# Kernel tuning notes

Measured on AMD Instinct MI355X. Metric: run time of the kernel, lower is better.

## Reference

```python
import jax, jax.numpy as jnp
import numpy as np

EMBD = 1024
N_HEADS = 16
DK = EMBD // N_HEADS


def setup_inputs() -> dict:
    key = jax.random.key(0)
    ks = jax.random.split(key, 5)
    B, T = 2, 2048
    scale = 1.0 / np.sqrt(EMBD)
    x = jax.random.normal(ks[0], (B, T, EMBD), dtype=jnp.float32)
    W_qkv = jax.random.normal(ks[1], (EMBD, 3 * EMBD), dtype=jnp.float32) * scale
    b_qkv = jnp.zeros((3 * EMBD,), dtype=jnp.float32)
    W_proj = jax.random.normal(ks[2], (EMBD, EMBD), dtype=jnp.float32) * scale
    b_proj = jnp.zeros((EMBD,), dtype=jnp.float32)
    return {"x": x, "W_qkv": W_qkv, "b_qkv": b_qkv, "W_proj": W_proj, "b_proj": b_proj}


def reference(x, W_qkv, b_qkv, W_proj, b_proj):
    B, T, C = x.shape
    qkv = x @ W_qkv + b_qkv                      # [B, T, 3C]
    q, k, v = jnp.split(qkv, 3, axis=-1)
    # [B, H, T, dk]
    q = q.reshape(B, T, N_HEADS, DK).transpose(0, 2, 1, 3)
    k = k.reshape(B, T, N_HEADS, DK).transpose(0, 2, 1, 3)
    v = v.reshape(B, T, N_HEADS, DK).transpose(0, 2, 1, 3)
    att = jnp.einsum('bhqd,bhkd->bhqk', q, k) / np.sqrt(DK).astype(np.float32)
    causal = jnp.triu(jnp.full((T, T), -jnp.inf, dtype=att.dtype), k=1)
    att = jax.nn.softmax(att + causal, axis=-1)  # dropout p=0.0 -> identity
    y = jnp.einsum('bhqk,bhkd->bhqd', att, v)    # [B, H, T, dk]
    y = y.transpose(0, 2, 1, 3).reshape(B, T, C)
    y = y @ W_proj + b_proj
    return (y, (k, v))
```

## Files before the change

### kernel.cpp

```cpp
#include <hip/hip_runtime.h>
#include <hip/hip_bf16.h>

#define B_   2
#define T_   2048
#define C_   1024
#define H_   16
#define DK_  64

typedef __bf16 bf16x8 __attribute__((ext_vector_type(8)));
typedef float  f32x4  __attribute__((ext_vector_type(4)));
typedef unsigned short u16;
typedef u16 u16x4 __attribute__((ext_vector_type(4)));
typedef u16 u16x8 __attribute__((ext_vector_type(8)));

static __device__ __forceinline__ u16 f2bf(float f) {
    unsigned u = __float_as_uint(f);
    u += 0x7fffu + ((u >> 16) & 1u);
    return (u16)(u >> 16);
}
static __device__ __forceinline__ float bf2f(u16 h) {
    return __uint_as_float(((unsigned)h) << 16);
}

static __device__ __forceinline__ void async16(void* l, const void* g) {
    __builtin_amdgcn_global_load_lds(
        (const __attribute__((address_space(1))) unsigned int*)g,
        (__attribute__((address_space(3))) unsigned int*)l, 16, 0, 0);
}

__global__ __launch_bounds__(256) void pack_a_hl(const float* __restrict__ src, char* __restrict__ dst) {
    const int mt = blockIdx.x, kt = blockIdx.y, t = threadIdx.x;
    const int r = t >> 1, half = t & 1;
    const float* s = src + (size_t)(mt * 128 + r) * 1024 + kt * 32 + half * 16;
    float f[16];
    #pragma unroll
    for (int i = 0; i < 4; ++i) *(float4*)&f[i * 4] = ((const float4*)s)[i];
    u16 hi[16] __attribute__((aligned(16))), lo[16] __attribute__((aligned(16)));
    #pragma unroll
    for (int e = 0; e < 16; ++e) { hi[e] = f2bf(f[e]); lo[e] = f2bf(f[e] - bf2f(hi[e])); }
    char* tb = dst + ((size_t)mt * 32 + kt) * 16384;
    const int sw = (r & 7) << 4;
    #pragma unroll
    for (int j = 0; j < 2; ++j) {
        int g = half * 2 + j;
        *(u16x8*)(tb + ((r * 128 + g * 16) ^ sw))      = *(u16x8*)&hi[j * 8];
        *(u16x8*)(tb + ((r * 128 + 64 + g * 16) ^ sw)) = *(u16x8*)&lo[j * 8];
    }
}

__global__ __launch_bounds__(256) void pack_a_s(const float* __restrict__ src, char* __restrict__ dst) {
    const int mt = blockIdx.x, kt = blockIdx.y, t = threadIdx.x;
    const int r = t >> 1, half = t & 1;
    const float* s = src + (size_t)(mt * 128 + r) * 1024 + kt * 64 + half * 32;
    float f[32];
    #pragma unroll
    for (int i = 0; i < 8; ++i) *(float4*)&f[i * 4] = ((const float4*)s)[i];
    u16 hv[32] __attribute__((aligned(16)));
    #pragma unroll
    for (int e = 0; e < 32; ++e) hv[e] = f2bf(f[e]);
    char* tb = dst + ((size_t)mt * 16 + kt) * 16384;
    const int sw = (r & 7) << 4;
    #pragma unroll
    for (int j = 0; j < 4; ++j) {
        int g = half * 4 + j;
        *(u16x8*)(tb + ((r * 128 + g * 16) ^ sw)) = *(u16x8*)&hv[j * 8];
    }
}

template <int BKT>
__global__ __launch_bounds__(256) void pack_bt_hl(const float* __restrict__ W, char* __restrict__ dst,
                                                  int N, int nkt) {
    __shared__ float Ls[BKT][132];
    const int nt = blockIdx.x, kt = blockIdx.y, t = threadIdx.x;
    #pragma unroll
    for (int p = 0; p < BKT / 32; ++p) {
        int kr = p * 32 + (t >> 3), c8 = t & 7;
        const float* s = W + (size_t)(kt * BKT + kr) * N + nt * 128 + c8 * 16;
        #pragma unroll
        for (int i = 0; i < 4; ++i) *(float4*)&Ls[kr][c8 * 16 + i * 4] = ((const float4*)s)[i];
    }
    __syncthreads();
    const int nr = t >> 1, half = t & 1;
    constexpr int KH = BKT / 2;
    constexpr int ROWB = BKT * 4;
    constexpr int TILEB = 128 * ROWB;
    char* tb = dst + ((size_t)nt * nkt + kt) * TILEB;
    u16 hi[KH] __attribute__((aligned(16))), lo[KH] __attribute__((aligned(16)));
    #pragma unroll
    for (int e = 0; e < KH; ++e) {
        float x = Ls[half * KH + e][nr];
        hi[e] = f2bf(x); lo[e] = f2bf(x - bf2f(hi[e]));
    }
    const int sw = (nr & 7) << 4;
    #pragma unroll
    for (int j = 0; j < KH / 8; ++j) {
        int g = half * (KH / 8) + j;
        *(u16x8*)(tb + ((nr * ROWB + g * 16) ^ sw))            = *(u16x8*)&hi[j * 8];
        *(u16x8*)(tb + ((nr * ROWB + ROWB / 2 + g * 16) ^ sw)) = *(u16x8*)&lo[j * 8];
    }
}

__global__ __launch_bounds__(256) void kv_pack(
    const float* __restrict__ k_in, const float* __restrict__ v_in,
    char* __restrict__ kp, char* __restrict__ vp)
{
    __shared__ float Ls[64][68];
    const int bh = blockIdx.x, kt = blockIdx.y, t = threadIdx.x;
    const float* Kb = k_in + (size_t)bh * T_ * DK_ + (size_t)kt * 64 * DK_;
    const float* Vb = v_in + (size_t)bh * T_ * DK_ + (size_t)kt * 64 * DK_;
    char* ktb = kp + ((size_t)bh * 32 + kt) * 16384;
    char* vtb = vp + ((size_t)bh * 32 + kt) * 16384;
    const int row = t >> 2, qtr = t & 3;

    {
        float f[16];
        #pragma unroll
        for (int i = 0; i < 4; ++i)
            *(float4*)&f[i * 4] = ((const float4*)(Kb + (size_t)row * 64 + qtr * 16))[i];
        u16 hi[16] __attribute__((aligned(16))), lo[16] __attribute__((aligned(16)));
        #pragma unroll
        for (int e = 0; e < 16; ++e) { hi[e] = f2bf(f[e]); lo[e] = f2bf(f[e] - bf2f(hi[e])); }
        const int sw = (row & 7) << 4;
        *(u16x8*)(ktb + ((row * 128 + qtr * 32) ^ sw))             = *(u16x8*)&hi[0];
        *(u16x8*)(ktb + ((row * 128 + qtr * 32 + 16) ^ sw))        = *(u16x8*)&hi[8];
        *(u16x8*)(ktb + 8192 + ((row * 128 + qtr * 32) ^ sw))      = *(u16x8*)&lo[0];
        *(u16x8*)(ktb + 8192 + ((row * 128 + qtr * 32 + 16) ^ sw)) = *(u16x8*)&lo[8];
    }

    #pragma unroll
    for (int i = 0; i < 4; ++i)
        *(float4*)&Ls[row][qtr * 16 + i * 4] = ((const float4*)(Vb + (size_t)row * 64 + qtr * 16))[i];
    __syncthreads();
    {
        const int dd = t >> 2, tc2 = t & 3;
        float f[16];
        #pragma unroll
        for (int k = 0; k < 16; ++k) f[k] = Ls[tc2 * 16 + k][dd];
        u16 hi[16] __attribute__((aligned(16))), lo[16] __attribute__((aligned(16)));
        #pragma unroll
        for (int e = 0; e < 16; ++e) { hi[e] = f2bf(f[e]); lo[e] = f2bf(f[e] - bf2f(hi[e])); }
        const int sw = (dd & 7) << 4;
        *(u16x8*)(vtb + ((dd * 128 + tc2 * 32) ^ sw))             = *(u16x8*)&hi[0];
        *(u16x8*)(vtb + ((dd * 128 + tc2 * 32 + 16) ^ sw))        = *(u16x8*)&hi[8];
        *(u16x8*)(vtb + 8192 + ((dd * 128 + tc2 * 32) ^ sw))      = *(u16x8*)&lo[0];
        *(u16x8*)(vtb + 8192 + ((dd * 128 + tc2 * 32 + 16) ^ sw)) = *(u16x8*)&lo[8];
    }
}

__global__ __launch_bounds__(256, 2) void qkv_gemm_bf16(
    const char* __restrict__ xp, const char* __restrict__ wqp,
    const float* __restrict__ bqkv,
    float* __restrict__ qy, float* __restrict__ k_out, float* __restrict__ v_out)
{
    __shared__ __align__(16) char Alds[16384];
    __shared__ __align__(16) char Blds[16384];
    const int mt = blockIdx.x, nt = blockIdx.y;
    const int t = threadIdx.x, lane = t & 63, w = t >> 6;
    const int g = lane >> 4, r15 = lane & 15;
    const int wm = w >> 1, wn = w & 1;

    int aoff[4][2], boff[4][2];
    #pragma unroll
    for (int s = 0; s < 4; ++s) {
        int ar = wm * 64 + s * 16 + r15, sa = (ar & 7) << 4;
        aoff[s][0] = (ar * 128 + g * 16) ^ sa;
        aoff[s][1] = (ar * 128 + 64 + g * 16) ^ sa;
        int br = wn * 64 + s * 16 + r15, sb = (br & 7) << 4;
        boff[s][0] = (br * 128 + g * 16) ^ sb;
        boff[s][1] = (br * 128 + 64 + g * 16) ^ sb;
    }

    f32x4 acc[4][4];
    #pragma unroll
    for (int i = 0; i < 4; ++i)
        #pragma unroll
        for (int j = 0; j < 4; ++j) acc[i][j] = (f32x4){0.f, 0.f, 0.f, 0.f};

    const char* Abase = xp + (size_t)mt * 32 * 16384 + w * 4096 + lane * 16;
    const char* Bbase = wqp + (size_t)nt * 32 * 16384 + w * 4096 + lane * 16;
    char* la = Alds + w * 4096;
    char* lb = Blds + w * 4096;

    for (int kt = 0; kt < 32; ++kt) {
        #pragma unroll
        for (int i = 0; i < 4; ++i) {
            async16(la + i * 1024, Abase + kt * 16384 + i * 1024);
            async16(lb + i * 1024, Bbase + kt * 16384 + i * 1024);
        }
        __syncthreads();
        bf16x8 af[4][2], bf[4][2];
        #pragma unroll
        for (int s = 0; s < 4; ++s) {
            af[s][0] = *(const bf16x8*)(Alds + aoff[s][0]);
            af[s][1] = *(const bf16x8*)(Alds + aoff[s][1]);
            bf[s][0] = *(const bf16x8*)(Blds + boff[s][0]);
            bf[s][1] = *(const bf16x8*)(Blds + boff[s][1]);
        }
        #pragma unroll
        for (int i = 0; i < 4; ++i)
            #pragma unroll
            for (int j = 0; j < 4; ++j) {
                acc[i][j] = __builtin_amdgcn_mfma_f32_16x16x32_bf16(af[i][0], bf[j][0], acc[i][j], 0, 0, 0);
                acc[i][j] = __builtin_amdgcn_mfma_f32_16x16x32_bf16(af[i][0], bf[j][1], acc[i][j], 0, 0, 0);
                acc[i][j] = __builtin_amdgcn_mfma_f32_16x16x32_bf16(af[i][1], bf[j][0], acc[i][j], 0, 0, 0);
            }
        __syncthreads();
    }

    const int n0 = nt * 128;
    const int sec = n0 >> 10;
    float* kv = (sec == 1) ? k_out : v_out;
    #pragma unroll
    for (int i = 0; i < 4; ++i) {
        int mbase = mt * 128 + wm * 64 + i * 16 + g * 4;
        #pragma unroll
        for (int j = 0; j < 4; ++j) {
            int n = n0 + wn * 64 + j * 16 + r15;
            float bias = bqkv[n];
            int c = n & 1023;
            #pragma unroll
            for (int r = 0; r < 4; ++r) {
                int m = mbase + r;
                int bb = m >> 11, tt = m & 2047;
                float val = acc[i][j][r] + bias;
                if (sec == 0)
                    qy[((size_t)bb * T_ + tt) * C_ + c] = val;
                else
                    kv[(((size_t)bb * H_ + (c >> 6)) * T_ + tt) * DK_ + (c & 63)] = val;
            }
        }
    }
}

__global__ __launch_bounds__(256, 2) void proj_gemm_bf16(
    const char* __restrict__ yap, const char* __restrict__ wpp,
    const float* __restrict__ bp, float* __restrict__ y)
{
    __shared__ __align__(16) char Alds[16384];
    __shared__ __align__(16) char Blds[32768];
    const int mt = blockIdx.x, nt = blockIdx.y;
    const int t = threadIdx.x, lane = t & 63, w = t >> 6;
    const int g = lane >> 4, r15 = lane & 15;
    const int wm = w >> 1, wn = w & 1;

    int aoff[4][2], boffh[4][2], boffl[4][2];
    #pragma unroll
    for (int s = 0; s < 4; ++s) {
        int ar = wm * 64 + s * 16 + r15, sa = (ar & 7) << 4;
        int br = wn * 64 + s * 16 + r15, sb = (br & 7) << 4;
        #pragma unroll
        for (int kk = 0; kk < 2; ++kk) {
            aoff[s][kk]  = (ar * 128 + (kk * 4 + g) * 16) ^ sa;
            boffh[s][kk] = (br * 256 + (kk * 4 + g) * 16) ^ sb;
            boffl[s][kk] = (br * 256 + 128 + (kk * 4 + g) * 16) ^ sb;
        }
    }

    f32x4 acc[4][4];
    #pragma unroll
    for (int i = 0; i < 4; ++i)
        #pragma unroll
        for (int j = 0; j < 4; ++j) acc[i][j] = (f32x4){0.f, 0.f, 0.f, 0.f};

    const char* Abase = yap + (size_t)mt * 16 * 16384 + w * 4096 + lane * 16;
    const char* Bbase = wpp + (size_t)nt * 16 * 32768 + w * 8192 + lane * 16;
    char* la = Alds + w * 4096;
    char* lb = Blds + w * 8192;

    for (int kt = 0; kt < 16; ++kt) {
        #pragma unroll
        for (int i = 0; i < 4; ++i)
            async16(la + i * 1024, Abase + kt * 16384 + i * 1024);
        #pragma unroll
        for (int i = 0; i < 8; ++i)
            async16(lb + i * 1024, Bbase + kt * 32768 + i * 1024);
        __syncthreads();
        #pragma unroll
        for (int kk = 0; kk < 2; ++kk) {
            bf16x8 af[4], bh[4], bl[4];
            #pragma unroll
            for (int s = 0; s < 4; ++s) {
                af[s] = *(const bf16x8*)(Alds + aoff[s][kk]);
                bh[s] = *(const bf16x8*)(Blds + boffh[s][kk]);
                bl[s] = *(const bf16x8*)(Blds + boffl[s][kk]);
            }
            #pragma unroll
            for (int i = 0; i < 4; ++i)
                #pragma unroll
                for (int j = 0; j < 4; ++j) {
                    acc[i][j] = __builtin_amdgcn_mfma_f32_16x16x32_bf16(af[i], bh[j], acc[i][j], 0, 0, 0);
                    acc[i][j] = __builtin_amdgcn_mfma_f32_16x16x32_bf16(af[i], bl[j], acc[i][j], 0, 0, 0);
                }
        }
        __syncthreads();
    }

    #pragma unroll
    for (int i = 0; i < 4; ++i) {
        int mbase = mt * 128 + wm * 64 + i * 16 + g * 4;
        #pragma unroll
        for (int j = 0; j < 4; ++j) {
            int n = nt * 128 + wn * 64 + j * 16 + r15;
            float bias = bp[n];
            #pragma unroll
            for (int r = 0; r < 4; ++r)
                y[(size_t)(mbase + r) * 1024 + n] = acc[i][j][r] + bias;
        }
    }
}

#define PS_H 0
#define PS_L 8192
#define KS_H 16384
#define KS_L 24576
#define VT_H 32768
#define VT_L 40960

__global__ __launch_bounds__(256) void attn_mfma_kernel(
    float* qyatt,
    const char* __restrict__ Kp,
    const char* __restrict__ Vp)
{
    __shared__ __align__(16) char lds[49152];

    const int bh   = blockIdx.x;
    const int qt   = 31 - (int)blockIdx.y;
    const int qb   = qt * 64;
    const int t    = threadIdx.x;
    const int lane = t & 63;
    const int w    = t >> 6;
    const int g    = lane >> 4;
    const int r15  = lane & 15;
    const int b    = bh >> 4, h = bh & 15;

    const float* Qb = qyatt + ((size_t)b * T_ + qb) * C_ + h * 64;

    #pragma unroll
    for (int di = 0; di < 4; ++di) {
        int fidx = di * 256 + t;
        int row  = fidx >> 4;
        int c4   = fidx & 15;
        float4 f = ((const float4*)(Qb + (size_t)row * C_))[c4];
        f.x *= 0.125f; f.y *= 0.125f; f.z *= 0.125f; f.w *= 0.125f;
        u16 h0 = f2bf(f.x), h1 = f2bf(f.y), h2 = f2bf(f.z), h3 = f2bf(f.w);
        u16 l0 = f2bf(f.x - bf2f(h0)), l1 = f2bf(f.y - bf2f(h1));
        u16 l2 = f2bf(f.z - bf2f(h2)), l3 = f2bf(f.w - bf2f(h3));
        int off = (row * 128 + c4 * 8) ^ ((row & 7) << 4);
        u16x4 hv = {h0, h1, h2, h3};
        u16x4 lv = {l0, l1, l2, l3};
        *(u16x4*)(lds + PS_H + off) = hv;
        *(u16x4*)(lds + PS_L + off) = lv;
    }
    __syncthreads();

    bf16x8 qfh[2], qfl[2];
    const int prow = w * 16 + r15;
    #pragma unroll
    for (int dc = 0; dc < 2; ++dc) {
        int off = (prow * 128 + dc * 64 + g * 16) ^ ((prow & 7) << 4);
        qfh[dc] = *(const bf16x8*)(lds + PS_H + off);
        qfl[dc] = *(const bf16x8*)(lds + PS_L + off);
    }

    f32x4 zero4 = {0.f, 0.f, 0.f, 0.f};
    f32x4 o[4];
    o[0] = zero4; o[1] = zero4; o[2] = zero4; o[3] = zero4;
    float mrun = -1e30f, lrun = 0.f;
    const int qglob = qb + w * 16 + r15;

    const int nt = qt + 1;
    for (int kt = 0; kt < nt; ++kt) {
        const int j0 = kt * 64;
        __syncthreads();
        {
            const char* Kg = Kp + ((size_t)bh * 32 + kt) * 16384 + w * 4096 + lane * 16;
            const char* Vg = Vp + ((size_t)bh * 32 + kt) * 16384 + w * 4096 + lane * 16;
            char* lk = lds + KS_H + w * 4096;
            char* lv = lds + VT_H + w * 4096;
            #pragma unroll
            for (int i = 0; i < 4; ++i) {
                async16(lk + i * 1024, Kg + i * 1024);
                async16(lv + i * 1024, Vg + i * 1024);
            }
        }
        __syncthreads();

        float sv[4][4];
        const bool diag = (kt == qt);
        #pragma unroll
        for (int st = 0; st < 4; ++st) {
            f32x4 acc = zero4;
            int krow = st * 16 + r15;
            #pragma unroll
            for (int dc = 0; dc < 2; ++dc) {
                int off = (krow * 128 + dc * 64 + g * 16) ^ ((krow & 7) << 4);
                bf16x8 kh = *(const bf16x8*)(lds + KS_H + off);
                bf16x8 kl = *(const bf16x8*)(lds + KS_L + off);
                acc = __builtin_amdgcn_mfma_f32_16x16x32_bf16(kh, qfh[dc], acc, 0, 0, 0);
                acc = __builtin_amdgcn_mfma_f32_16x16x32_bf16(kh, qfl[dc], acc, 0, 0, 0);
                acc = __builtin_amdgcn_mfma_f32_16x16x32_bf16(kl, qfh[dc], acc, 0, 0, 0);
            }
            #pragma unroll
            for (int r = 0; r < 4; ++r) {
                float x = acc[r];
                if (diag) {
                    int kg = j0 + st * 16 + g * 4 + r;
                    if (kg > qglob) x = -1e30f;
                }
                sv[st][r] = x;
            }
        }

        float tm = sv[0][0];
        #pragma unroll
        for (int st = 0; st < 4; ++st)
            #pragma unroll
            for (int r = 0; r < 4; ++r) tm = fmaxf(tm, sv[st][r]);
        tm = fmaxf(tm, __shfl_xor(tm, 16));
        tm = fmaxf(tm, __shfl_xor(tm, 32));
        float mnew = fmaxf(mrun, tm);
        float resc = __expf(mrun - mnew);
        mrun = mnew;
        lrun *= resc;
        o[0] *= resc; o[1] *= resc; o[2] *= resc; o[3] *= resc;

        float ps = 0.f;
        #pragma unroll
        for (int st = 0; st < 4; ++st)
            #pragma unroll
            for (int r = 0; r < 4; ++r) {
                float p = __expf(sv[st][r] - mnew);
                sv[st][r] = p;
                ps += p;
            }
        ps += __shfl_xor(ps, 16);
        ps += __shfl_xor(ps, 32);
        lrun += ps;

        #pragma unroll
        for (int st = 0; st < 4; ++st) {
            u16 h0 = f2bf(sv[st][0]), h1 = f2bf(sv[st][1]);
            u16 h2 = f2bf(sv[st][2]), h3 = f2bf(sv[st][3]);
            u16 l0 = f2bf(sv[st][0] - bf2f(h0)), l1 = f2bf(sv[st][1] - bf2f(h1));
            u16 l2 = f2bf(sv[st][2] - bf2f(h2)), l3 = f2bf(sv[st][3] - bf2f(h3));
            int off = (prow * 128 + (st * 16 + g * 4) * 2) ^ ((prow & 7) << 4);
            u16x4 hv = {h0, h1, h2, h3};
            u16x4 lv = {l0, l1, l2, l3};
            *(u16x4*)(lds + PS_H + off) = hv;
            *(u16x4*)(lds + PS_L + off) = lv;
        }

        bf16x8 pfh[2], pfl[2];
        #pragma unroll
        for (int kc = 0; kc < 2; ++kc) {
            int off = (prow * 128 + kc * 64 + g * 16) ^ ((prow & 7) << 4);
            pfh[kc] = *(const bf16x8*)(lds + PS_H + off);
            pfl[kc] = *(const bf16x8*)(lds + PS_L + off);
        }
        #pragma unroll
        for (int dt = 0; dt < 4; ++dt) {
            int vrow = dt * 16 + r15;
            #pragma unroll
            for (int kc = 0; kc < 2; ++kc) {
                int off = (vrow * 128 + kc * 64 + g * 16) ^ ((vrow & 7) << 4);
                bf16x8 vh = *(const bf16x8*)(lds + VT_H + off);
                bf16x8 vl = *(const bf16x8*)(lds + VT_L + off);
                o[dt] = __builtin_amdgcn_mfma_f32_16x16x32_bf16(vh, pfh[kc], o[dt], 0, 0, 0);
                o[dt] = __builtin_amdgcn_mfma_f32_16x16x32_bf16(vh, pfl[kc], o[dt], 0, 0, 0);
                o[dt] = __builtin_amdgcn_mfma_f32_16x16x32_bf16(vl, pfh[kc], o[dt], 0, 0, 0);
            }
        }
    }

    const float inv = 1.f / lrun;
    float* yo = qyatt + ((size_t)b * T_ + qglob) * C_ + h * DK_;
    #pragma unroll
    for (int dt = 0; dt < 4; ++dt)
        #pragma unroll
        for (int r = 0; r < 4; ++r)
            yo[dt * 16 + g * 4 + r] = o[dt][r] * inv;
}

extern "C" void kernel_launch(void* const* d_in, const int* in_sizes, int n_in,
                              void* d_out, int out_size, void* d_ws, size_t ws_size,
                              hipStream_t stream) {
    const float* x     = (const float*)d_in[0];
    const float* Wqkv  = (const float*)d_in[1];
    const float* bqkv  = (const float*)d_in[2];
    const float* Wproj = (const float*)d_in[3];
    const float* bproj = (const float*)d_in[4];

    float* y     = (float*)d_out;
    float* k_out = y + (size_t)4194304;
    float* v_out = y + (size_t)8388608;

    char* ws = (char*)d_ws;
    char* xp  = ws;
    char* wqp = ws + ((size_t)16 << 20);
    char* Kp  = ws;
    char* Vp  = ws + ((size_t)16 << 20);
    char* yap = ws;
    char* wpp = ws + ((size_t)8 << 20);

    pack_a_hl     <<<dim3(32, 32), 256, 0, stream>>>(x, xp);
    pack_bt_hl<32><<<dim3(24, 32), 256, 0, stream>>>(Wqkv, wqp, 3072, 32);
    qkv_gemm_bf16 <<<dim3(32, 24), 256, 0, stream>>>(xp, wqp, bqkv, y, k_out, v_out);
    kv_pack       <<<dim3(32, 32), 256, 0, stream>>>(k_out, v_out, Kp, Vp);
    attn_mfma_kernel<<<dim3(32, 32), 256, 0, stream>>>(y, Kp, Vp);
    pack_a_s      <<<dim3(32, 16), 256, 0, stream>>>(y, yap);
    pack_bt_hl<64><<<dim3(8, 16), 256, 0, stream>>>(Wproj, wpp, 1024, 16);
    proj_gemm_bf16<<<dim3(32, 8), 256, 0, stream>>>(yap, wpp, bproj, y);
}
```

Measured before the change: 292.0 us.

## Use single bf16 for P, exp2 softmax, lazy rescale, smaller LDS

Drops the split hi/lo bf16 representation of the softmax probabilities, so the P·V product needs two MFMAs per step instead of three and half the P LDS traffic. The log2(e) factor is folded into the Q scale so exp2f replaces __expf, and the running-max rescale is skipped unless the tile max exceeds the current max by a threshold. LDS shrinks from 48KB to 40KB by reusing the K high buffer for the Q low part, which may raise occupancy. Risks: lower precision in P and bounded growth of unnormalised exponentials from the lazy rescale.

```diff
diff --git a/kernel.cpp b/kernel.cpp
--- a/kernel.cpp
+++ b/kernel.cpp
@@ -8,6 +8,7 @@
 #define DK_  64
 
 typedef __bf16 bf16x8 __attribute__((ext_vector_type(8)));
+typedef __bf16 bf16x4v __attribute__((ext_vector_type(4)));
 typedef float  f32x4  __attribute__((ext_vector_type(4)));
 typedef unsigned short u16;
 typedef u16 u16x4 __attribute__((ext_vector_type(4)));
@@ -309,19 +310,18 @@
     }
 }
 
-#define PS_H 0
-#define PS_L 8192
-#define KS_H 16384
-#define KS_L 24576
-#define VT_H 32768
-#define VT_L 40960
+#define PS_   0
+#define KS_H  8192
+#define KS_L  16384
+#define VT_H  24576
+#define VT_L  32768
 
 __global__ __launch_bounds__(256) void attn_mfma_kernel(
     float* qyatt,
     const char* __restrict__ Kp,
     const char* __restrict__ Vp)
 {
-    __shared__ __align__(16) char lds[49152];
+    __shared__ __align__(16) char lds[40960];
 
     const int bh   = blockIdx.x;
     const int qt   = 31 - (int)blockIdx.y;
@@ -334,6 +334,7 @@
     const int b    = bh >> 4, h = bh & 15;
 
     const float* Qb = qyatt + ((size_t)b * T_ + qb) * C_ + h * 64;
+    const float QSCALE = 0.125f * 1.44269504088896f;
 
     #pragma unroll
     for (int di = 0; di < 4; ++di) {
@@ -341,15 +342,15 @@
         int row  = fidx >> 4;
         int c4   = fidx & 15;
         float4 f = ((const float4*)(Qb + (size_t)row * C_))[c4];
-        f.x *= 0.125f; f.y *= 0.125f; f.z *= 0.125f; f.w *= 0.125f;
+        f.x *= QSCALE; f.y *= QSCALE; f.z *= QSCALE; f.w *= QSCALE;
         u16 h0 = f2bf(f.x), h1 = f2bf(f.y), h2 = f2bf(f.z), h3 = f2bf(f.w);
         u16 l0 = f2bf(f.x - bf2f(h0)), l1 = f2bf(f.y - bf2f(h1));
         u16 l2 = f2bf(f.z - bf2f(h2)), l3 = f2bf(f.w - bf2f(h3));
         int off = (row * 128 + c4 * 8) ^ ((row & 7) << 4);
         u16x4 hv = {h0, h1, h2, h3};
         u16x4 lv = {l0, l1, l2, l3};
-        *(u16x4*)(lds + PS_H + off) = hv;
-        *(u16x4*)(lds + PS_L + off) = lv;
+        *(u16x4*)(lds + PS_  + off) = hv;
+        *(u16x4*)(lds + KS_H + off) = lv;
     }
     __syncthreads();
 
@@ -358,8 +359,8 @@
     #pragma unroll
     for (int dc = 0; dc < 2; ++dc) {
         int off = (prow * 128 + dc * 64 + g * 16) ^ ((prow & 7) << 4);
-        qfh[dc] = *(const bf16x8*)(lds + PS_H + off);
-        qfl[dc] = *(const bf16x8*)(lds + PS_L + off);
+        qfh[dc] = *(const bf16x8*)(lds + PS_  + off);
+        qfl[dc] = *(const bf16x8*)(lds + KS_H + off);
     }
 
     f32x4 zero4 = {0.f, 0.f, 0.f, 0.f};
@@ -418,18 +419,20 @@
             for (int r = 0; r < 4; ++r) tm = fmaxf(tm, sv[st][r]);
         tm = fmaxf(tm, __shfl_xor(tm, 16));
         tm = fmaxf(tm, __shfl_xor(tm, 32));
-        float mnew = fmaxf(mrun, tm);
-        float resc = __expf(mrun - mnew);
-        mrun = mnew;
-        lrun *= resc;
-        o[0] *= resc; o[1] *= resc; o[2] *= resc; o[3] *= resc;
+        if (__any(tm > mrun + 11.5f)) {
+            float mnew = fmaxf(mrun, tm);
+            float resc = exp2f(mrun - mnew);
+            mrun = mnew;
+            lrun *= resc;
+            o[0] *= resc; o[1] *= resc; o[2] *= resc; o[3] *= resc;
+        }
 
         float ps = 0.f;
         #pragma unroll
         for (int st = 0; st < 4; ++st)
             #pragma unroll
             for (int r = 0; r < 4; ++r) {
-                float p = __expf(sv[st][r] - mnew);
+                float p = exp2f(sv[st][r] - mrun);
                 sv[st][r] = p;
                 ps += p;
             }
@@ -439,23 +442,17 @@
 
         #pragma unroll
         for (int st = 0; st < 4; ++st) {
-            u16 h0 = f2bf(sv[st][0]), h1 = f2bf(sv[st][1]);
-            u16 h2 = f2bf(sv[st][2]), h3 = f2bf(sv[st][3]);
-            u16 l0 = f2bf(sv[st][0] - bf2f(h0)), l1 = f2bf(sv[st][1] - bf2f(h1));
-            u16 l2 = f2bf(sv[st][2] - bf2f(h2)), l3 = f2bf(sv[st][3] - bf2f(h3));
+            bf16x4v pb = { (__bf16)sv[st][0], (__bf16)sv[st][1],
+                           (__bf16)sv[st][2], (__bf16)sv[st][3] };
             int off = (prow * 128 + (st * 16 + g * 4) * 2) ^ ((prow & 7) << 4);
-            u16x4 hv = {h0, h1, h2, h3};
-            u16x4 lv = {l0, l1, l2, l3};
-            *(u16x4*)(lds + PS_H + off) = hv;
-            *(u16x4*)(lds + PS_L + off) = lv;
-        }
-
-        bf16x8 pfh[2], pfl[2];
+            *(bf16x4v*)(lds + PS_ + off) = pb;
+        }
+
+        bf16x8 pf[2];
         #pragma unroll
         for (int kc = 0; kc < 2; ++kc) {
             int off = (prow * 128 + kc * 64 + g * 16) ^ ((prow & 7) << 4);
-            pfh[kc] = *(const bf16x8*)(lds + PS_H + off);
-            pfl[kc] = *(const bf16x8*)(lds + PS_L + off);
+            pf[kc] = *(const bf16x8*)(lds + PS_ + off);
         }
         #pragma unroll
         for (int dt = 0; dt < 4; ++dt) {
@@ -465,9 +462,8 @@
                 int off = (vrow * 128 + kc * 64 + g * 16) ^ ((vrow & 7) << 4);
                 bf16x8 vh = *(const bf16x8*)(lds + VT_H + off);
                 bf16x8 vl = *(const bf16x8*)(lds + VT_L + off);
-                o[dt] = __builtin_amdgcn_mfma_f32_16x16x32_bf16(vh, pfh[kc], o[dt], 0, 0, 0);
-                o[dt] = __builtin_amdgcn_mfma_f32_16x16x32_bf16(vh, pfl[kc], o[dt], 0, 0, 0);
-                o[dt] = __builtin_amdgcn_mfma_f32_16x16x32_bf16(vl, pfh[kc], o[dt], 0, 0, 0);
+                o[dt] = __builtin_amdgcn_mfma_f32_16x16x32_bf16(vh, pf[kc], o[dt], 0, 0, 0);
+                o[dt] = __builtin_amdgcn_mfma_f32_16x16x32_bf16(vl, pf[kc], o[dt], 0, 0, 0);
             }
         }
     }
```

New measurement: 298.7 us. 2.3% more time.
